# Optimization experiments

Measured on AMD Instinct MI355X. Metric: run time of the kernel, lower is better.

The kernel has to match this reference:

```python
import jax, jax.numpy as jnp
import numpy as np

# model dims
B_, S_, D_ = 2, 2048, 1024
D_STATE, EXPAND, HEADDIM, CHUNK, NGROUPS = 128, 2, 64, 64, 1
D_INNER = EXPAND * D_
NHEADS = D_INNER // HEADDIM  # 32 ssd heads
D_PROJ = 2 * D_INNER + 2 * NGROUPS * D_STATE + NHEADS  # 4384
H_, KV_, HD_ = 16, 4, 64  # attention heads / kv heads / head dim
ROPE_DIMS = 16
MLP_DIM = int(3.0 * D_)


def _rmsnorm(x, w=None, eps=1e-5):
    y = x * jax.lax.rsqrt(jnp.mean(x * x, axis=-1, keepdims=True) + eps)
    return y * w if w is not None else y


def _layernorm(x, w, b, eps=1e-5):
    m = jnp.mean(x, axis=-1, keepdims=True)
    v = jnp.mean((x - m) ** 2, axis=-1, keepdims=True)
    return (x - m) * jax.lax.rsqrt(v + eps) * w + b


def _segsum(x):
    # (..., T) -> (..., T, T) lower-tri cumulative sums, -inf above diag
    T = x.shape[-1]
    i = jnp.arange(T)
    xx = jnp.where(i[:, None] > i[None, :], jnp.broadcast_to(x[..., None], x.shape + (T,)), 0.0)
    s = jnp.cumsum(xx, axis=-2)
    return jnp.where(i[:, None] >= i[None, :], s, -jnp.inf)


def _ssd_chunked(x, A, B, C, chunk):
    # x:(b,s,h,p) A:(b,s,h) B,C:(b,s,g,n)
    b, s, h, p = x.shape
    g, n = B.shape[2], B.shape[3]
    if g < h:
        B = jnp.repeat(B, h // g, axis=2)
        C = jnp.repeat(C, h // g, axis=2)
    c = s // chunk
    x = x.reshape(b, c, chunk, h, p)
    A = A.reshape(b, c, chunk, h).transpose(0, 3, 1, 2)  # b h c l
    B = B.reshape(b, c, chunk, h, n)
    C = C.reshape(b, c, chunk, h, n)
    L = jnp.exp(_segsum(A))
    Y_diag = jnp.einsum('bclhn,bcshn,bhcls,bcshp->bclhp', C, B, L, x)
    A_cum = jnp.cumsum(A, axis=-1)
    decay_states = jnp.exp(A_cum[..., -1:] - A_cum)
    states = jnp.einsum('bclhn,bhcl,bclhp->bchpn', B, decay_states, x)
    decay_chunk = jnp.exp(_segsum(jnp.pad(A_cum[..., -1], ((0, 0), (0, 0), (1, 0)))))
    new_states = jnp.einsum('bhzc,bchpn->bzhpn', decay_chunk[:, :, :c, 1:c + 1], states)
    Y_off = jnp.einsum('bclhn,bchpn,bhcl->bclhp', C, new_states, jnp.exp(A_cum))
    return (Y_diag + Y_off).reshape(b, s, h, p)


def _rope_cos_sin(s, rd, base=10000.0):
    inv = 1.0 / base ** (jnp.arange(0, rd, 2, dtype=jnp.float32) / rd)
    f = jnp.outer(jnp.arange(s, dtype=jnp.float32), inv)  # (s, rd/2)
    return jnp.cos(f)[None, :, None, :], jnp.sin(f)[None, :, None, :]


def _apply_rope(x, cos, sin, rd):
    xr, xp = x[..., :rd], x[..., rd:]
    half = rd // 2
    x1, x2 = xr[..., :half], xr[..., half:]
    xr = jnp.concatenate([x1 * cos + x2 * sin, -x1 * sin + x2 * cos], axis=-1)
    return jnp.concatenate([xr, xp], axis=-1)


def _mamba_block(x, mnorm_w, in_w, out_w, Dp, dt_b, A_log, Bn_w, Cn_w):
    b, s, _ = x.shape
    h = _rmsnorm(x, mnorm_w)
    zxbcdt = h @ in_w.T
    z, xs, Bc, Cc, dt = jnp.split(
        zxbcdt,
        [D_INNER, 2 * D_INNER, 2 * D_INNER + NGROUPS * D_STATE, 2 * D_INNER + 2 * NGROUPS * D_STATE],
        axis=-1)
    dt = jax.nn.softplus(dt + dt_b)  # (b,s,nheads)
    A = -jnp.exp(A_log)  # (nheads,)
    xs = xs.reshape(b, s, NHEADS, HEADDIM)
    Bc = _rmsnorm(Bc.reshape(b, s, NGROUPS, D_STATE), Bn_w)
    Cc = _rmsnorm(Cc.reshape(b, s, NGROUPS, D_STATE), Cn_w)
    y = _ssd_chunked(xs * dt[..., None], A[None, None, :] * dt, Bc, Cc, CHUNK)
    y = y + xs * Dp[None, None, :, None]
    y = y * jax.nn.silu(z).reshape(b, s, NHEADS, HEADDIM)
    return x + y.reshape(b, s, D_INNER) @ out_w.T


def _attn_block(x, ln1_w, ln1_b, cq_w, ck_w, cv_w, cproj_w, q_gain, ln2_w, ln2_b, fc_w, proj_w):
    b, s, d = x.shape
    h = _layernorm(x, ln1_w, ln1_b)
    q = (h @ cq_w.T).reshape(b, s, H_, HD_)
    k = (h @ ck_w.T).reshape(b, s, KV_, HD_)
    v = (h @ cv_w.T).reshape(b, s, KV_, HD_)
    eps = jnp.finfo(x.dtype).eps
    q = _rmsnorm(q, eps=eps)
    k = _rmsnorm(k, eps=eps)
    cos, sin = _rope_cos_sin(s, ROPE_DIMS)
    q = _apply_rope(q, cos, sin, ROPE_DIMS)
    k = _apply_rope(k, cos, sin, ROPE_DIMS)
    q = q * q_gain[None, None, :, None]
    rep = H_ // KV_
    k = jnp.repeat(k, rep, axis=2)
    v = jnp.repeat(v, rep, axis=2)
    scores = jnp.einsum('bqhd,bkhd->bhqk', q, k) / np.float32(np.sqrt(HD_))
    i = jnp.arange(s)
    scores = jnp.where(i[:, None] >= i[None, :], scores, -jnp.inf)
    w = jax.nn.softmax(scores, axis=-1)
    y = jnp.einsum('bhqk,bkhd->bqhd', w, v).reshape(b, s, d)
    x = x + y @ cproj_w.T
    h = _layernorm(x, ln2_w, ln2_b)
    return x + jax.nn.silu(h @ fc_w.T) @ proj_w.T


def setup_inputs() -> dict:
    key = jax.random.key(0)
    ks = jax.random.split(key, 16)
    rn = lambda k, shp, sc=0.02: (jax.random.normal(k, shp, dtype=jnp.float32) * sc)
    return {
        'x': jax.random.normal(ks[0], (B_, S_, D_), dtype=jnp.float32),
        'mnorm_w': jnp.ones((D_,), jnp.float32),
        'in_proj_w': rn(ks[1], (D_PROJ, D_)),
        'out_proj_w': rn(ks[2], (D_, D_INNER)),
        'D_param': jnp.ones((NHEADS,), jnp.float32),
        'dt_bias': rn(ks[3], (NHEADS,), 0.1),
        'A_log': jnp.log(0.5 + jax.random.uniform(ks[4], (NHEADS,), dtype=jnp.float32) * 0.5),
        'Bn_w': jnp.ones((D_STATE,), jnp.float32),
        'Cn_w': jnp.ones((D_STATE,), jnp.float32),
        'ln1_w': jnp.ones((D_,), jnp.float32),
        'ln1_b': jnp.zeros((D_,), jnp.float32),
        'cq_w': rn(ks[5], (D_, D_)),
        'ck_w': rn(ks[6], (KV_ * HD_, D_)),
        'cv_w': rn(ks[7], (KV_ * HD_, D_)),
        'cproj_w': rn(ks[8], (D_, D_)),
        'q_gain': jnp.full((H_,), 5.25, jnp.float32),
        'ln2_w': jnp.ones((D_,), jnp.float32),
        'ln2_b': jnp.zeros((D_,), jnp.float32),
        'fc_w': rn(ks[9], (MLP_DIM, D_)),
        'proj_w': rn(ks[10], (D_, MLP_DIM)),
    }


def reference(x, mnorm_w, in_proj_w, out_proj_w, D_param, dt_bias, A_log, Bn_w, Cn_w,
              ln1_w, ln1_b, cq_w, ck_w, cv_w, cproj_w, q_gain, ln2_w, ln2_b, fc_w, proj_w):
    x = _mamba_block(x, mnorm_w, in_proj_w, out_proj_w, D_param, dt_bias, A_log, Bn_w, Cn_w)
    x = _attn_block(x, ln1_w, ln1_b, cq_w, ck_w, cv_w, cproj_w, q_gain, ln2_w, ln2_b, fc_w, proj_w)
    return x
```

## Files before the change

kernel.cpp:

```cpp
#include <hip/hip_runtime.h>
#include <hip/hip_bf16.h>
#include <math.h>

#define B_    2
#define S_    2048
#define D_    1024
#define DI    2048
#define NH    32
#define HD    64
#define DS    128
#define CH    64
#define NC    32
#define DP    4384
#define HATT  16
#define KVH   4
#define RD    16
#define MLP   3072
#define ROWS  (B_*S_)

typedef __bf16 bf16;
typedef __bf16 bf16x8 __attribute__((ext_vector_type(8)));
typedef __bf16 bf16x4 __attribute__((ext_vector_type(4)));
typedef float  f32x4  __attribute__((ext_vector_type(4)));

__device__ __forceinline__ void async_copy16(const void* g, void* l) {
  __builtin_amdgcn_global_load_lds(
      (const __attribute__((address_space(1))) unsigned int*)g,
      (__attribute__((address_space(3))) unsigned int*)l, 16, 0, 0);
}

__device__ __forceinline__ float waveReduceSum(float v) {
#pragma unroll
  for (int off = 32; off > 0; off >>= 1) v += __shfl_down(v, off, 64);
  return v;
}

template<int NW>
__device__ __forceinline__ float blockReduceSum(float v, float* sh) {
  v = waveReduceSum(v);
  int lane = threadIdx.x & 63, wid = threadIdx.x >> 6;
  if (lane == 0) sh[wid] = v;
  __syncthreads();
  float s = 0.f;
#pragma unroll
  for (int i = 0; i < NW; i++) s += sh[i];
  __syncthreads();
  return s;
}

struct CastSeg { const float* src; bf16* dst; int nval; int ntot; int blk0; };
struct CastArgs { CastSeg seg[8]; };

__global__ __launch_bounds__(256) void castw_all(CastArgs a) {
  int blk = blockIdx.x;
  int si = 0;
#pragma unroll
  for (int i = 1; i < 8; i++) if (blk >= a.seg[i].blk0) si = i;
  CastSeg s = a.seg[si];
  int i = ((blk - s.blk0) * 256 + threadIdx.x) * 4;
  if (i >= s.ntot) return;
  float4 v = {0.f, 0.f, 0.f, 0.f};
  if (i < s.nval) v = *(const float4*)(s.src + i);
  bf16x4 o;
  o[0] = (bf16)v.x; o[1] = (bf16)v.y; o[2] = (bf16)v.z; o[3] = (bf16)v.w;
  *(bf16x4*)(s.dst + i) = o;
}

__global__ __launch_bounds__(256) void rmsnorm_k(const float* __restrict__ x,
                                                 const float* __restrict__ w,
                                                 bf16* __restrict__ y, int n) {
  __shared__ float sh[4];
  size_t row = blockIdx.x;
  const float* xr = x + row * n;
  bf16* yr = y + row * n;
  float ss = 0.f;
  for (int i = threadIdx.x; i < n; i += 256) { float v = xr[i]; ss += v * v; }
  ss = blockReduceSum<4>(ss, sh);
  float inv = rsqrtf(ss / n + 1e-5f);
  for (int i = threadIdx.x; i < n; i += 256) yr[i] = (bf16)(xr[i] * inv * w[i]);
}

template<int ACT, typename OT>
__global__ __launch_bounds__(256) void gemm_mfma(const bf16* __restrict__ A,
                                                 const bf16* __restrict__ W,
                                                 const float* __restrict__ R,
                                                 OT* __restrict__ C,
                                                 int M, int N, int K) {
  __shared__ bf16 As[128 * 32];
  __shared__ bf16 Ws[128 * 32];
  int tid = threadIdx.x, lane = tid & 63, wave = tid >> 6;
  int bm = blockIdx.y * 128, bn = blockIdx.x * 128;
  const bf16* gA0 = A + (size_t)(bm + wave * 32 + (lane >> 2)) * K + (lane & 3) * 8;
  const bf16* gA1 = gA0 + (size_t)16 * K;
  const bf16* gW0 = W + (size_t)(bn + wave * 32 + (lane >> 2)) * K + (lane & 3) * 8;
  const bf16* gW1 = gW0 + (size_t)16 * K;
  bf16* lA0 = As + wave * 32 * 32;
  bf16* lA1 = lA0 + 16 * 32;
  bf16* lW0 = Ws + wave * 32 * 32;
  bf16* lW1 = lW0 + 16 * 32;
  int fr = lane & 15, fq = lane >> 4;
  int wm = wave >> 1, wn = wave & 1;
  const bf16* pA = As + (wm * 64 + fr) * 32 + fq * 8;
  const bf16* pW = Ws + (wn * 64 + fr) * 32 + fq * 8;
  f32x4 acc[4][4] = {};
  for (int k0 = 0; k0 < K; k0 += 32) {
    async_copy16(gA0, lA0);
    async_copy16(gA1, lA1);
    async_copy16(gW0, lW0);
    async_copy16(gW1, lW1);
    gA0 += 32; gA1 += 32; gW0 += 32; gW1 += 32;
    __syncthreads();
    bf16x8 af[4], bfr[4];
#pragma unroll
    for (int mi = 0; mi < 4; mi++) af[mi] = *(const bf16x8*)(pA + mi * 16 * 32);
#pragma unroll
    for (int ni = 0; ni < 4; ni++) bfr[ni] = *(const bf16x8*)(pW + ni * 16 * 32);
#pragma unroll
    for (int mi = 0; mi < 4; mi++)
#pragma unroll
      for (int ni = 0; ni < 4; ni++)
        acc[mi][ni] = __builtin_amdgcn_mfma_f32_16x16x32_bf16(af[mi], bfr[ni], acc[mi][ni], 0, 0, 0);
    __syncthreads();
  }
#pragma unroll
  for (int mi = 0; mi < 4; mi++) {
    int row = bm + wm * 64 + mi * 16 + fq * 4;
#pragma unroll
    for (int ni = 0; ni < 4; ni++) {
      int col = bn + wn * 64 + ni * 16 + fr;
      if (col < N) {
#pragma unroll
        for (int r = 0; r < 4; r++) {
          float v = acc[mi][ni][r];
          if (ACT == 1) v = v / (1.f + __expf(-v));
          if (R) v += R[(size_t)(row + r) * N + col];
          C[(size_t)(row + r) * N + col] = (OT)v;
        }
      }
    }
  }
}

__global__ __launch_bounds__(256) void gemm_sk(const bf16* __restrict__ A,
                                               const bf16* __restrict__ W,
                                               float* __restrict__ P,
                                               int M, int N, int K, int kchunk) {
  __shared__ bf16 As[128 * 32];
  __shared__ bf16 Ws[128 * 32];
  int tid = threadIdx.x, lane = tid & 63, wave = tid >> 6;
  int bm = blockIdx.y * 128, bn = blockIdx.x * 128;
  int ks = blockIdx.z;
  int kbeg = ks * kchunk;
  const bf16* gA0 = A + (size_t)(bm + wave * 32 + (lane >> 2)) * K + kbeg + (lane & 3) * 8;
  const bf16* gA1 = gA0 + (size_t)16 * K;
  const bf16* gW0 = W + (size_t)(bn + wave * 32 + (lane >> 2)) * K + kbeg + (lane & 3) * 8;
  const bf16* gW1 = gW0 + (size_t)16 * K;
  bf16* lA0 = As + wave * 32 * 32;
  bf16* lA1 = lA0 + 16 * 32;
  bf16* lW0 = Ws + wave * 32 * 32;
  bf16* lW1 = lW0 + 16 * 32;
  int fr = lane & 15, fq = lane >> 4;
  int wm = wave >> 1, wn = wave & 1;
  const bf16* pA = As + (wm * 64 + fr) * 32 + fq * 8;
  const bf16* pW = Ws + (wn * 64 + fr) * 32 + fq * 8;
  f32x4 acc[4][4] = {};
  for (int k0 = 0; k0 < kchunk; k0 += 32) {
    async_copy16(gA0, lA0);
    async_copy16(gA1, lA1);
    async_copy16(gW0, lW0);
    async_copy16(gW1, lW1);
    gA0 += 32; gA1 += 32; gW0 += 32; gW1 += 32;
    __syncthreads();
    bf16x8 af[4], bfr[4];
#pragma unroll
    for (int mi = 0; mi < 4; mi++) af[mi] = *(const bf16x8*)(pA + mi * 16 * 32);
#pragma unroll
    for (int ni = 0; ni < 4; ni++) bfr[ni] = *(const bf16x8*)(pW + ni * 16 * 32);
#pragma unroll
    for (int mi = 0; mi < 4; mi++)
#pragma unroll
      for (int ni = 0; ni < 4; ni++)
        acc[mi][ni] = __builtin_amdgcn_mfma_f32_16x16x32_bf16(af[mi], bfr[ni], acc[mi][ni], 0, 0, 0);
    __syncthreads();
  }
  float* Pp = P + (size_t)ks * M * N;
#pragma unroll
  for (int mi = 0; mi < 4; mi++) {
    int row = bm + wm * 64 + mi * 16 + fq * 4;
#pragma unroll
    for (int ni = 0; ni < 4; ni++) {
      int col = bn + wn * 64 + ni * 16 + fr;
#pragma unroll
      for (int r = 0; r < 4; r++)
        Pp[(size_t)(row + r) * N + col] = acc[mi][ni][r];
    }
  }
}

__global__ __launch_bounds__(256) void reduce_ln2(const float* __restrict__ p0,
                                                  const float* __restrict__ p1,
                                                  const float* __restrict__ res,
                                                  const float* __restrict__ w,
                                                  const float* __restrict__ b,
                                                  float* __restrict__ xo,
                                                  bf16* __restrict__ ho) {
  __shared__ float buf[1024];
  __shared__ float sh[4];
  size_t o = (size_t)blockIdx.x * 1024;
  float s = 0.f, s2 = 0.f;
  for (int i = threadIdx.x; i < 1024; i += 256) {
    float v = p0[o + i] + p1[o + i] + res[o + i];
    buf[i] = v; s += v; s2 += v * v;
  }
  s  = blockReduceSum<4>(s,  sh);
  s2 = blockReduceSum<4>(s2, sh);
  float mean = s / 1024.f;
  float var  = s2 / 1024.f - mean * mean;
  float inv  = rsqrtf(var + 1e-5f);
  for (int i = threadIdx.x; i < 1024; i += 256) {
    float v = buf[i];
    xo[o + i] = v;
    ho[o + i] = (bf16)((v - mean) * inv * w[i] + b[i]);
  }
}

__global__ __launch_bounds__(256) void reduce_out3(const float* __restrict__ p0,
                                                   const float* __restrict__ p1,
                                                   const float* __restrict__ p2,
                                                   const float* __restrict__ res,
                                                   float* __restrict__ out) {
  int i = (blockIdx.x * 256 + threadIdx.x) * 4;
  f32x4 v = *(const f32x4*)(p0 + i);
  v += *(const f32x4*)(p1 + i);
  v += *(const f32x4*)(p2 + i);
  v += *(const f32x4*)(res + i);
  *(f32x4*)(out + i) = v;
}

__global__ __launch_bounds__(256) void reduce_qkv(const float* __restrict__ P,
                                                  const float* __restrict__ q_gain,
                                                  bf16* __restrict__ q,
                                                  bf16* __restrict__ k,
                                                  bf16* __restrict__ v) {
  __shared__ float buf[1536];
  size_t row = blockIdx.x;
  size_t o = row * 1536;
  const float* p0 = P + o;
  const float* p1 = P + (size_t)ROWS * 1536 + o;
  int tid = threadIdx.x;
  for (int i = tid; i < 384; i += 256) {
    f32x4 a = *(const f32x4*)(p0 + i * 4);
    f32x4 c = *(const f32x4*)(p1 + i * 4);
    *(f32x4*)(buf + i * 4) = a + c;
  }
  __syncthreads();
  int lane = tid & 63, w = tid >> 6;
  int s = (int)(row & (S_ - 1));
  int ri = lane & 7;
  float rinv = __expf(-(float)ri * (0.125f * 9.210340371976184f));
  float ang = (float)s * rinv;
  float cs = cosf(ang), sn = sinf(ang);
#pragma unroll
  for (int j = 0; j < 6; j++) {
    int hh = w * 6 + j;
    float val = buf[hh * 64 + lane];
    if (hh < 20) {
      float ss = val * val;
#pragma unroll
      for (int off = 32; off > 0; off >>= 1) ss += __shfl_xor(ss, off, 64);
      val *= rsqrtf(ss / 64.f + 1.1920929e-7f);
      float other = __shfl_xor(val, 8, 64);
      float res = val;
      if (lane < RD) res = (lane < 8) ? (val * cs + other * sn) : (val * cs - other * sn);
      if (hh < 16) {
        res *= q_gain[hh];
        q[row * (HATT * HD) + hh * HD + lane] = (bf16)res;
      } else {
        k[row * (KVH * HD) + (hh - 16) * HD + lane] = (bf16)res;
      }
    } else {
      v[row * (KVH * HD) + (hh - 20) * HD + lane] = (bf16)val;
    }
  }
}

__global__ __launch_bounds__(256) void gemm_inproj(const bf16* __restrict__ A,
                                                   const bf16* __restrict__ W,
                                                   bf16* __restrict__ zt,
                                                   bf16* __restrict__ xt,
                                                   bf16* __restrict__ bcdt) {
  const int K = 1024;
  __shared__ bf16 As[128 * 32];
  __shared__ bf16 Ws[128 * 32];
  int tid = threadIdx.x, lane = tid & 63, wave = tid >> 6;
  int bm = blockIdx.y * 128, bn = blockIdx.x * 128;
  const bf16* gA0 = A + (size_t)(bm + wave * 32 + (lane >> 2)) * K + (lane & 3) * 8;
  const bf16* gA1 = gA0 + (size_t)16 * K;
  const bf16* gW0 = W + (size_t)(bn + wave * 32 + (lane >> 2)) * K + (lane & 3) * 8;
  const bf16* gW1 = gW0 + (size_t)16 * K;
  bf16* lA0 = As + wave * 32 * 32;
  bf16* lA1 = lA0 + 16 * 32;
  bf16* lW0 = Ws + wave * 32 * 32;
  bf16* lW1 = lW0 + 16 * 32;
  int fr = lane & 15, fq = lane >> 4;
  int wm = wave >> 1, wn = wave & 1;
  const bf16* pA = As + (wm * 64 + fr) * 32 + fq * 8;
  const bf16* pW = Ws + (wn * 64 + fr) * 32 + fq * 8;
  f32x4 acc[4][4] = {};
  for (int k0 = 0; k0 < K; k0 += 32) {
    async_copy16(gA0, lA0);
    async_copy16(gA1, lA1);
    async_copy16(gW0, lW0);
    async_copy16(gW1, lW1);
    gA0 += 32; gA1 += 32; gW0 += 32; gW1 += 32;
    __syncthreads();
    bf16x8 af[4], bfr[4];
#pragma unroll
    for (int mi = 0; mi < 4; mi++) af[mi] = *(const bf16x8*)(pA + mi * 16 * 32);
#pragma unroll
    for (int ni = 0; ni < 4; ni++) bfr[ni] = *(const bf16x8*)(pW + ni * 16 * 32);
#pragma unroll
    for (int mi = 0; mi < 4; mi++)
#pragma unroll
      for (int ni = 0; ni < 4; ni++)
        acc[mi][ni] = __builtin_amdgcn_mfma_f32_16x16x32_bf16(af[mi], bfr[ni], acc[mi][ni], 0, 0, 0);
    __syncthreads();
  }
#pragma unroll
  for (int mi = 0; mi < 4; mi++) {
    int row0m = bm + wm * 64 + mi * 16 + fq * 4;
    int b = row0m >> 11, sg = row0m & 2047;
#pragma unroll
    for (int ni = 0; ni < 4; ni++) {
      int col = bn + wn * 64 + ni * 16 + fr;
      bf16x4 o;
#pragma unroll
      for (int r = 0; r < 4; r++) o[r] = (bf16)acc[mi][ni][r];
      if (col < 2048) {
        *(bf16x4*)(zt + ((size_t)(b * NH + (col >> 6)) * HD + (col & 63)) * S_ + sg) = o;
      } else if (col < 4096) {
        int xc = col - 2048;
        *(bf16x4*)(xt + ((size_t)(b * NH + (xc >> 6)) * HD + (xc & 63)) * S_ + sg) = o;
      } else if (col < 4384) {
#pragma unroll
        for (int r = 0; r < 4; r++)
          bcdt[(size_t)(row0m + r) * 288 + (col - 4096)] = o[r];
      }
    }
  }
}

__global__ __launch_bounds__(256) void t64(const bf16* __restrict__ in, bf16* __restrict__ out,
                                           int istr, size_t io, size_t oo, int n_nt) {
  __shared__ bf16 T[64 * 72];
  int bid = blockIdx.x;
  int st = bid & 31;
  int nt = (bid >> 5) % n_nt;
  int outer = bid / (32 * n_nt);
  const bf16* ip = in + outer * io + (size_t)st * 64 * istr + nt * 64;
  int tid = threadIdx.x;
#pragma unroll
  for (int i = 0; i < 2; i++) {
    int cid = tid + i * 256; int s = cid >> 3, pc = (cid & 7) * 8;
    *(bf16x8*)(T + s * 72 + pc) = *(const bf16x8*)(ip + (size_t)s * istr + pc);
  }
  __syncthreads();
  bf16* op = out + outer * oo + (size_t)nt * 64 * 2048 + st * 64;
#pragma unroll
  for (int i = 0; i < 2; i++) {
    int cid = tid + i * 256; int p = cid >> 3, sc = (cid & 7) * 8;
    bf16x8 o;
#pragma unroll
    for (int j = 0; j < 8; j++) o[j] = T[(sc + j) * 72 + p];
    *(bf16x8*)(op + (size_t)p * 2048 + sc) = o;
  }
}

__global__ __launch_bounds__(64) void ssd_prep(const bf16* __restrict__ bcdt,
                                               const float* __restrict__ dt_bias,
                                               const float* __restrict__ A_log,
                                               float* __restrict__ dt_c,
                                               float* __restrict__ ddc,
                                               float* __restrict__ ac_c,
                                               float* __restrict__ T_out) {
  int bid = blockIdx.x;
  int c = bid % NC, hh = (bid / NC) % NH, b = bid / (NC * NH);
  int l = threadIdx.x;
  size_t row = (size_t)b * S_ + c * 64 + l;
  float raw = (float)bcdt[row * 288 + 256 + hh] + dt_bias[hh];
  float dtv = (raw > 20.f) ? raw : log1pf(__expf(raw));
  float a = -__expf(A_log[hh]) * dtv;
  float ps = a;
#pragma unroll
  for (int off = 1; off < 64; off <<= 1) {
    float t = __shfl_up(ps, off, 64);
    if (l >= off) ps += t;
  }
  float a63 = __shfl(ps, 63, 64);
  size_t o = ((size_t)b * NH + hh) * S_ + c * 64 + l;
  dt_c[o] = dtv;
  ac_c[o] = ps;
  ddc[o] = __expf(a63 - ps) * dtv;
  if (l == 63) T_out[(b * NH + hh) * NC + c] = ps;
}

__global__ __launch_bounds__(128) void bc_norm(const bf16* __restrict__ bcdt,
                                               const float* __restrict__ Bw,
                                               const float* __restrict__ Cw,
                                               bf16* __restrict__ Bn,
                                               bf16* __restrict__ Cn) {
  __shared__ float shb[2], shc[2];
  size_t row = blockIdx.x;
  int i = threadIdx.x;
  float bv = (float)bcdt[row * 288 + i];
  float cv = (float)bcdt[row * 288 + 128 + i];
  float sb = waveReduceSum(bv * bv);
  float sc = waveReduceSum(cv * cv);
  int lane = threadIdx.x & 63, wid = threadIdx.x >> 6;
  if (lane == 0) { shb[wid] = sb; shc[wid] = sc; }
  __syncthreads();
  float tb = shb[0] + shb[1];
  float tc = shc[0] + shc[1];
  Bn[row * DS + i] = (bf16)(bv * rsqrtf(tb / DS + 1e-5f) * Bw[i]);
  Cn[row * DS + i] = (bf16)(cv * rsqrtf(tc / DS + 1e-5f) * Cw[i]);
}

__global__ __launch_bounds__(256) void ssd_states(const bf16* __restrict__ Xt,
                                                  const bf16* __restrict__ Btr,
                                                  const float* __restrict__ ddc,
                                                  float* __restrict__ states) {
  __shared__ bf16 Xs[64 * 72];
  __shared__ bf16 Bs[128 * 72];
  int bid = blockIdx.x;
  int h = bid % NH;
  int c = (bid / NH) % NC;
  int b = bid / (NH * NC);
  int tid = threadIdx.x, lane = tid & 63, w = tid >> 6;
  int fr = lane & 15, fq = lane >> 4;
  const size_t xbase = (size_t)(b * NH + h) * HD * S_ + c * 64;
  const size_t dbase = (size_t)(b * NH + h) * S_ + c * 64;
#pragma unroll
  for (int i = 0; i < 2; i++) {
    int cid = tid + i * 256; int p = cid >> 3, sc = (cid & 7) * 8;
    bf16x8 xv = *(const bf16x8*)(Xt + xbase + (size_t)p * S_ + sc);
    f32x4 d0 = *(const f32x4*)(ddc + dbase + sc);
    f32x4 d1 = *(const f32x4*)(ddc + dbase + sc + 4);
    bf16x8 o;
#pragma unroll
    for (int j = 0; j < 4; j++) { o[j] = (bf16)((float)xv[j] * d0[j]); o[4 + j] = (bf16)((float)xv[4 + j] * d1[j]); }
    *(bf16x8*)(Xs + p * 72 + sc) = o;
  }
  const size_t bbase = (size_t)b * 128 * S_ + c * 64;
#pragma unroll
  for (int i = 0; i < 4; i++) {
    int cid = tid + i * 256; int n = cid >> 3, sc = (cid & 7) * 8;
    *(bf16x8*)(Bs + n * 72 + sc) = *(const bf16x8*)(Btr + bbase + (size_t)n * S_ + sc);
  }
  __syncthreads();
  f32x4 acc[4][2] = {};
#pragma unroll
  for (int ks = 0; ks < 2; ks++) {
    bf16x8 a[4], bb[2];
#pragma unroll
    for (int pt = 0; pt < 4; pt++) a[pt] = *(const bf16x8*)(Xs + (pt * 16 + fr) * 72 + ks * 32 + fq * 8);
#pragma unroll
    for (int n2 = 0; n2 < 2; n2++) bb[n2] = *(const bf16x8*)(Bs + ((2 * w + n2) * 16 + fr) * 72 + ks * 32 + fq * 8);
#pragma unroll
    for (int pt = 0; pt < 4; pt++)
#pragma unroll
      for (int n2 = 0; n2 < 2; n2++)
        acc[pt][n2] = __builtin_amdgcn_mfma_f32_16x16x32_bf16(a[pt], bb[n2], acc[pt][n2], 0, 0, 0);
  }
  float* outp = states + (size_t)bid * 8192;
#pragma unroll
  for (int pt = 0; pt < 4; pt++)
#pragma unroll
    for (int n2 = 0; n2 < 2; n2++) {
      int n = (2 * w + n2) * 16 + fr;
#pragma unroll
      for (int r = 0; r < 4; r++)
        outp[(size_t)(pt * 16 + fq * 4 + r) * 128 + n] = acc[pt][n2][r];
    }
}

__global__ __launch_bounds__(256) void ssd_scan(float* __restrict__ states,
                                                const float* __restrict__ T) {
  __shared__ float eT[NC];
  int part = blockIdx.x & 7;
  int bh = blockIdx.x >> 3;
  int b = bh / NH, h = bh % NH;
  if (threadIdx.x < NC) eT[threadIdx.x] = __expf(T[(size_t)(b * NH + h) * NC + threadIdx.x]);
  __syncthreads();
  const size_t cstride = (size_t)NH * HD * DS;
  size_t base = ((size_t)b * NC * NH + h) * (HD * DS);
#pragma unroll
  for (int j = 0; j < 4; j++) {
    int e = part * 1024 + threadIdx.x + j * 256;
    float carry = 0.f;
    size_t idx = base + e;
    for (int c = 0; c < NC; c++) {
      float sv = states[idx];
      states[idx] = carry;
      carry = sv + eT[c] * carry;
      idx += cstride;
    }
  }
}

__global__ __launch_bounds__(256) void ssd_out(const bf16* __restrict__ Cn,
                                               const bf16* __restrict__ Bn,
                                               const bf16* __restrict__ Xt,
                                               const bf16* __restrict__ Zt,
                                               const float* __restrict__ dt_c,
                                               const float* __restrict__ ac_c,
                                               const float* __restrict__ states,
                                               const float* __restrict__ Dp,
                                               bf16* __restrict__ ybf) {
  __shared__ bf16 Cs[64 * 136];
  __shared__ bf16 BNs[64 * 136];
  __shared__ bf16 Xs[64 * 72];
  __shared__ bf16 G[64 * 72];
  __shared__ float acs[64];
  int bid = blockIdx.x;
  int h = bid % NH;
  int c = (bid / NH) % NC;
  int b = bid / (NH * NC);
  int tid = threadIdx.x, lane = tid & 63, w = tid >> 6;
  int fr = lane & 15, fq = lane >> 4;
  size_t row0 = (size_t)b * S_ + c * 64;
  const size_t abase = (size_t)(b * NH + h) * S_ + c * 64;
  if (tid < 64) acs[tid] = ac_c[abase + tid];
#pragma unroll
  for (int i = 0; i < 4; i++) {
    int cid = tid + i * 256; int l = cid >> 4, nc = (cid & 15) * 8;
    float e = __expf(ac_c[abase + l]);
    bf16x8 cv = *(const bf16x8*)(Cn + (row0 + l) * DS + nc);
    bf16x8 o;
#pragma unroll
    for (int j = 0; j < 8; j++) o[j] = (bf16)((float)cv[j] * e);
    *(bf16x8*)(Cs + l * 136 + nc) = o;
    *(bf16x8*)(BNs + l * 136 + nc) = *(const bf16x8*)(Bn + (row0 + l) * DS + nc);
  }
  const size_t xbase = (size_t)(b * NH + h) * HD * S_ + c * 64;
#pragma unroll
  for (int i = 0; i < 2; i++) {
    int cid = tid + i * 256; int p = cid >> 3, sc = (cid & 7) * 8;
    bf16x8 xv = *(const bf16x8*)(Xt + xbase + (size_t)p * S_ + sc);
    f32x4 d0 = *(const f32x4*)(dt_c + abase + sc);
    f32x4 d1 = *(const f32x4*)(dt_c + abase + sc + 4);
    bf16x8 o;
#pragma unroll
    for (int j = 0; j < 4; j++) { o[j] = (bf16)((float)xv[j] * d0[j]); o[4 + j] = (bf16)((float)xv[4 + j] * d1[j]); }
    *(bf16x8*)(Xs + p * 72 + sc) = o;
  }
  __syncthreads();
  bf16x8 ca[4];
#pragma unroll
  for (int ks = 0; ks < 4; ks++) ca[ks] = *(const bf16x8*)(Cs + (w * 16 + fr) * 136 + ks * 32 + fq * 8);
  f32x4 cb[4] = {};
  for (int st = 0; st <= w; st++)
#pragma unroll
    for (int ks = 0; ks < 4; ks++)
      cb[st] = __builtin_amdgcn_mfma_f32_16x16x32_bf16(ca[ks],
                 *(const bf16x8*)(BNs + (st * 16 + fr) * 136 + ks * 32 + fq * 8), cb[st], 0, 0, 0);
#pragma unroll
  for (int st = 0; st < 4; st++) {
    float es = (st <= w) ? __expf(-acs[st * 16 + fr]) : 0.f;
#pragma unroll
    for (int r = 0; r < 4; r++) {
      int lloc = fq * 4 + r;
      float g = 0.f;
      if (st < w) g = cb[st][r] * es;
      else if (st == w) g = (lloc >= fr) ? cb[st][r] * es : 0.f;
      G[(w * 16 + lloc) * 72 + st * 16 + fr] = (bf16)g;
    }
  }
  f32x4 acc[4] = {};
  {
    bf16x8 ga0 = *(const bf16x8*)(G + (w * 16 + fr) * 72 + fq * 8);
    bf16x8 ga1 = *(const bf16x8*)(G + (w * 16 + fr) * 72 + 32 + fq * 8);
#pragma unroll
    for (int pt = 0; pt < 4; pt++) {
      acc[pt] = __builtin_amdgcn_mfma_f32_16x16x32_bf16(ga0,
                  *(const bf16x8*)(Xs + (pt * 16 + fr) * 72 + fq * 8), acc[pt], 0, 0, 0);
      acc[pt] = __builtin_amdgcn_mfma_f32_16x16x32_bf16(ga1,
                  *(const bf16x8*)(Xs + (pt * 16 + fr) * 72 + 32 + fq * 8), acc[pt], 0, 0, 0);
    }
  }
  __syncthreads();
  const float* stp = states + (size_t)bid * 8192;
#pragma unroll
  for (int i = 0; i < 4; i++) {
    int cid = tid + i * 256; int p = cid >> 4, nc = (cid & 15) * 8;
    f32x4 s0 = *(const f32x4*)(stp + (size_t)p * 128 + nc);
    f32x4 s1 = *(const f32x4*)(stp + (size_t)p * 128 + nc + 4);
    bf16x8 o;
#pragma unroll
    for (int j = 0; j < 4; j++) { o[j] = (bf16)s0[j]; o[4 + j] = (bf16)s1[j]; }
    *(bf16x8*)(BNs + p * 136 + nc) = o;
  }
  __syncthreads();
#pragma unroll
  for (int pt = 0; pt < 4; pt++)
#pragma unroll
    for (int ks = 0; ks < 4; ks++)
      acc[pt] = __builtin_amdgcn_mfma_f32_16x16x32_bf16(ca[ks],
                  *(const bf16x8*)(BNs + (pt * 16 + fr) * 136 + ks * 32 + fq * 8), acc[pt], 0, 0, 0);
  float dph = Dp[h];
#pragma unroll
  for (int pt = 0; pt < 4; pt++) {
    int p = pt * 16 + fr;
    size_t tb = (xbase + (size_t)p * S_) + w * 16 + fq * 4;
    bf16x4 xs4 = *(const bf16x4*)(Xt + tb);
    bf16x4 z4  = *(const bf16x4*)(Zt + tb);
#pragma unroll
    for (int r = 0; r < 4; r++) {
      int l = w * 16 + fq * 4 + r;
      float yv = acc[pt][r] + (float)xs4[r] * dph;
      float z = (float)z4[r];
      yv *= z / (1.f + __expf(-z));
      ybf[((row0 + l) * NH + h) * HD + p] = (bf16)yv;
    }
  }
}

#define KSTR 72
#define PSTR 80
__global__ __launch_bounds__(256) void attn_mfma(const bf16* __restrict__ q,
                                                 const bf16* __restrict__ k,
                                                 const bf16* __restrict__ vtr,
                                                 bf16* __restrict__ o) {
  __shared__ bf16 Ks[2][64 * KSTR];
  __shared__ bf16 Vs[2][64 * KSTR];
  __shared__ bf16 Pl[4 * 16 * PSTR];
  int qt = (gridDim.x - 1) - blockIdx.x;
  int h = blockIdx.y, b = blockIdx.z;
  int kvh = h >> 2;
  int tid = threadIdx.x, lane = tid & 63, w = tid >> 6;
  int fr = lane & 15, fq = lane >> 4;
  const float SC = 0.18033688011112042f;
  const float M2 = 62.0f;
  const bf16* qp = q + (size_t)(b * S_ + qt * 64 + w * 16 + fr) * (HATT * HD) + h * HD + fq * 8;
  bf16x8 bq0 = *(const bf16x8*)(qp);
  bf16x8 bq1 = *(const bf16x8*)(qp + 32);
  int sr = tid >> 3, sc8 = (tid & 7) * 8;
  const bf16* kg = k + ((size_t)(b * S_) + sr) * (KVH * HD) + kvh * HD + sc8;
  const bf16* vg = vtr + ((size_t)(b * KVH + kvh) * HD + sr) * S_ + sc8;
  bf16x8 krg0, krg1, vrg0, vrg1;
  {
    const bf16* kp = kg;
    const bf16* vp = vg;
    krg0 = *(const bf16x8*)(kp);
    krg1 = *(const bf16x8*)(kp + (size_t)32 * (KVH * HD));
    vrg0 = *(const bf16x8*)(vp);
    vrg1 = *(const bf16x8*)(vp + (size_t)32 * S_);
    *(bf16x8*)(&Ks[0][sr * KSTR + sc8]) = krg0;
    *(bf16x8*)(&Ks[0][(sr + 32) * KSTR + sc8]) = krg1;
    *(bf16x8*)(&Vs[0][sr * KSTR + sc8]) = vrg0;
    *(bf16x8*)(&Vs[0][(sr + 32) * KSTR + sc8]) = vrg1;
  }
  float lsum = 0.f;
  f32x4 yacc[4] = {};
  bf16* Plw = Pl + w * 16 * PSTR;
  for (int kt = 0; kt <= qt; kt++) {
    int cur = kt & 1;
    bool more = kt < qt;
    if (more) {
      const bf16* kp = kg + (size_t)(kt + 1) * 64 * (KVH * HD);
      const bf16* vp = vg + (size_t)(kt + 1) * 64;
      krg0 = *(const bf16x8*)(kp);
      krg1 = *(const bf16x8*)(kp + (size_t)32 * (KVH * HD));
      vrg0 = *(const bf16x8*)(vp);
      vrg1 = *(const bf16x8*)(vp + (size_t)32 * S_);
    }
    __syncthreads();
    bool diag = (kt == qt);
#pragma unroll
    for (int mi = 0; mi < 4; mi++) {
      bf16x4 pk = {};
      if (!diag || mi <= w) {
        const bf16* krow = &Ks[cur][(mi * 16 + fr) * KSTR + fq * 8];
        bf16x8 ak0 = *(const bf16x8*)(krow);
        bf16x8 ak1 = *(const bf16x8*)(krow + 32);
        f32x4 s = {};
        s = __builtin_amdgcn_mfma_f32_16x16x32_bf16(ak0, bq0, s, 0, 0, 0);
        s = __builtin_amdgcn_mfma_f32_16x16x32_bf16(ak1, bq1, s, 0, 0, 0);
#pragma unroll
        for (int r = 0; r < 4; r++) {
          bool ok = !diag || (mi < w) || (fq * 4 + r <= fr);
          float p = ok ? __builtin_amdgcn_exp2f(s[r] * SC - M2) : 0.f;
          lsum += p;
          pk[r] = (bf16)p;
        }
      }
      *(bf16x4*)(Plw + fr * PSTR + mi * 16 + fq * 4) = pk;
    }
    bf16x8 bp0 = *(const bf16x8*)(Plw + fr * PSTR + fq * 8);
    bool hi = !diag || (w >= 2);
    bf16x8 bp1 = {};
    if (hi) bp1 = *(const bf16x8*)(Plw + fr * PSTR + 32 + fq * 8);
#pragma unroll
    for (int pi = 0; pi < 4; pi++) {
      const bf16* vrow = &Vs[cur][(pi * 16 + fr) * KSTR + fq * 8];
      bf16x8 av0 = *(const bf16x8*)(vrow);
      yacc[pi] = __builtin_amdgcn_mfma_f32_16x16x32_bf16(av0, bp0, yacc[pi], 0, 0, 0);
      if (hi) {
        bf16x8 av1 = *(const bf16x8*)(vrow + 32);
        yacc[pi] = __builtin_amdgcn_mfma_f32_16x16x32_bf16(av1, bp1, yacc[pi], 0, 0, 0);
      }
    }
    if (more) {
      int nxt = cur ^ 1;
      *(bf16x8*)(&Ks[nxt][sr * KSTR + sc8]) = krg0;
      *(bf16x8*)(&Ks[nxt][(sr + 32) * KSTR + sc8]) = krg1;
      *(bf16x8*)(&Vs[nxt][sr * KSTR + sc8]) = vrg0;
      *(bf16x8*)(&Vs[nxt][(sr + 32) * KSTR + sc8]) = vrg1;
    }
  }
  lsum += __shfl_xor(lsum, 16, 64);
  lsum += __shfl_xor(lsum, 32, 64);
  float inv = 1.f / lsum;
  bf16* op = o + (size_t)(b * S_ + qt * 64 + w * 16 + fr) * (HATT * HD) + h * HD + fq * 4;
#pragma unroll
  for (int pi = 0; pi < 4; pi++) {
    bf16x4 ov;
#pragma unroll
    for (int r = 0; r < 4; r++) ov[r] = (bf16)(yacc[pi][r] * inv);
    *(bf16x4*)(op + pi * 16) = ov;
  }
}

constexpr size_t OFF_WIN  = 0;
constexpr size_t OFF_WOUT = 9175040;
constexpr size_t OFF_WQKV = 13369344;
constexpr size_t OFF_WCP  = 16515072;
constexpr size_t OFF_WFC  = 18612224;
constexpr size_t OFF_WPR  = 24903680;
constexpr size_t OFF_HBF  = 31195136;
constexpr size_t OFF_BCDT = 39583744;
constexpr size_t OFF_XT   = 41943040;
constexpr size_t OFF_ZT   = 58720256;
constexpr size_t OFF_DTC  = 75497472;
constexpr size_t OFF_DDC  = 76546048;
constexpr size_t OFF_ACC  = 77594624;
constexpr size_t OFF_T    = 78643200;
constexpr size_t OFF_BN   = 78651392;
constexpr size_t OFF_CN   = 79699968;
constexpr size_t OFF_BTR  = 80748544;
constexpr size_t OFF_ST   = 81797120;
constexpr size_t OFF_YBF  = 148905984;
constexpr size_t OFF_X1   = 165683200;
constexpr size_t OFF_P    = OFF_ST;
constexpr size_t OFF_QB   = OFF_ST + 50331648;
constexpr size_t OFF_KB   = OFF_ST + 58720256;
constexpr size_t OFF_VB   = OFF_ST + 60817408;
constexpr size_t OFF_VTR  = OFF_ST + 62914560;
constexpr size_t OFF_Y2   = OFF_XT;
constexpr size_t OFF_X2   = 50331648;
constexpr size_t OFF_MLP  = 132128768;

extern "C" void kernel_launch(void* const* d_in, const int* in_sizes, int n_in,
                              void* d_out, int out_size, void* d_ws, size_t ws_size,
                              hipStream_t stream) {
  (void)in_sizes; (void)n_in; (void)out_size; (void)ws_size;
  const float* x        = (const float*)d_in[0];
  const float* mnorm_w  = (const float*)d_in[1];
  const float* in_w     = (const float*)d_in[2];
  const float* out_w    = (const float*)d_in[3];
  const float* Dp       = (const float*)d_in[4];
  const float* dt_bias  = (const float*)d_in[5];
  const float* A_log    = (const float*)d_in[6];
  const float* Bn_w     = (const float*)d_in[7];
  const float* Cn_w     = (const float*)d_in[8];
  const float* ln1_w    = (const float*)d_in[9];
  const float* ln1_b    = (const float*)d_in[10];
  const float* cq_w     = (const float*)d_in[11];
  const float* ck_w     = (const float*)d_in[12];
  const float* cv_w     = (const float*)d_in[13];
  const float* cproj_w  = (const float*)d_in[14];
  const float* q_gain   = (const float*)d_in[15];
  const float* ln2_w    = (const float*)d_in[16];
  const float* ln2_b    = (const float*)d_in[17];
  const float* fc_w     = (const float*)d_in[18];
  const float* proj_w   = (const float*)d_in[19];
  float* out = (float*)d_out;
  char* W8 = (char*)d_ws;

  bf16* w_in   = (bf16*)(W8 + OFF_WIN);
  bf16* w_out  = (bf16*)(W8 + OFF_WOUT);
  bf16* w_qkv  = (bf16*)(W8 + OFF_WQKV);
  bf16* w_cp   = (bf16*)(W8 + OFF_WCP);
  bf16* w_fc   = (bf16*)(W8 + OFF_WFC);
  bf16* w_pr   = (bf16*)(W8 + OFF_WPR);
  bf16* h_bf   = (bf16*)(W8 + OFF_HBF);
  bf16* bcdt   = (bf16*)(W8 + OFF_BCDT);
  bf16* Xt     = (bf16*)(W8 + OFF_XT);
  bf16* Zt     = (bf16*)(W8 + OFF_ZT);
  float* dt_c  = (float*)(W8 + OFF_DTC);
  float* ddc   = (float*)(W8 + OFF_DDC);
  float* ac_c  = (float*)(W8 + OFF_ACC);
  float* Tb    = (float*)(W8 + OFF_T);
  bf16* Bn     = (bf16*)(W8 + OFF_BN);
  bf16* Cn     = (bf16*)(W8 + OFF_CN);
  bf16* Btr    = (bf16*)(W8 + OFF_BTR);
  float* st    = (float*)(W8 + OFF_ST);
  bf16* ybf    = (bf16*)(W8 + OFF_YBF);
  float* x1    = (float*)(W8 + OFF_X1);
  float* Pbuf  = (float*)(W8 + OFF_P);
  bf16* qbf    = (bf16*)(W8 + OFF_QB);
  bf16* kbf    = (bf16*)(W8 + OFF_KB);
  bf16* vbf    = (bf16*)(W8 + OFF_VB);
  bf16* vtr    = (bf16*)(W8 + OFF_VTR);
  bf16* y2     = (bf16*)(W8 + OFF_Y2);
  float* x2    = (float*)(W8 + OFF_X2);
  bf16* mlp    = (bf16*)(W8 + OFF_MLP);

  CastArgs ca;
  ca.seg[0] = { in_w,    w_in,            4489216, 4587520, 0     };
  ca.seg[1] = { out_w,   w_out,           2097152, 2097152, 4480  };
  ca.seg[2] = { cq_w,    w_qkv,           1048576, 1048576, 6528  };
  ca.seg[3] = { ck_w,    w_qkv + 1048576,  262144,  262144, 7552  };
  ca.seg[4] = { cv_w,    w_qkv + 1310720,  262144,  262144, 7808  };
  ca.seg[5] = { cproj_w, w_cp,            1048576, 1048576, 8064  };
  ca.seg[6] = { fc_w,    w_fc,            3145728, 3145728, 9088  };
  ca.seg[7] = { proj_w,  w_pr,            3145728, 3145728, 12160 };
  castw_all<<<15232, 256, 0, stream>>>(ca);

  const size_t PS = (size_t)ROWS * 1024;

  rmsnorm_k<<<ROWS, 256, 0, stream>>>(x, mnorm_w, h_bf, D_);
  gemm_inproj<<<dim3(35, 32), 256, 0, stream>>>(h_bf, w_in, Zt, Xt, bcdt);
  ssd_prep<<<B_ * NH * NC, 64, 0, stream>>>(bcdt, dt_bias, A_log, dt_c, ddc, ac_c, Tb);
  bc_norm<<<ROWS, 128, 0, stream>>>(bcdt, Bn_w, Cn_w, Bn, Cn);
  t64<<<2 * 2 * 32, 256, 0, stream>>>(Bn, Btr, 128, (size_t)2048 * 128, (size_t)128 * 2048, 2);
  ssd_states<<<B_ * NC * NH, 256, 0, stream>>>(Xt, Btr, ddc, st);
  ssd_scan<<<B_ * NH * 8, 256, 0, stream>>>(st, Tb);
  ssd_out<<<B_ * NC * NH, 256, 0, stream>>>(Cn, Bn, Xt, Zt, dt_c, ac_c, st, Dp, ybf);
  gemm_sk<<<dim3(8, 32, 2), 256, 0, stream>>>(ybf, w_out, Pbuf, ROWS, D_, DI, 1024);
  reduce_ln2<<<ROWS, 256, 0, stream>>>(Pbuf, Pbuf + PS, x, ln1_w, ln1_b, x1, h_bf);

  gemm_sk<<<dim3(12, 32, 2), 256, 0, stream>>>(h_bf, w_qkv, Pbuf, ROWS, 1536, D_, 512);
  reduce_qkv<<<ROWS, 256, 0, stream>>>(Pbuf, q_gain, qbf, kbf, vbf);
  t64<<<2 * 4 * 32, 256, 0, stream>>>(vbf, vtr, 256, (size_t)2048 * 256, (size_t)256 * 2048, 4);
  attn_mfma<<<dim3(S_ / 64, HATT, B_), 256, 0, stream>>>(qbf, kbf, vtr, y2);
  gemm_sk<<<dim3(8, 32, 2), 256, 0, stream>>>(y2, w_cp, Pbuf, ROWS, D_, D_, 512);
  reduce_ln2<<<ROWS, 256, 0, stream>>>(Pbuf, Pbuf + PS, x1, ln2_w, ln2_b, x2, h_bf);

  gemm_mfma<1, bf16><<<dim3(24, 32), 256, 0, stream>>>(h_bf, w_fc, nullptr, mlp, ROWS, MLP, D_);
  gemm_sk<<<dim3(8, 32, 3), 256, 0, stream>>>(mlp, w_pr, Pbuf, ROWS, D_, MLP, 1024);
  reduce_out3<<<ROWS, 256, 0, stream>>>(Pbuf, Pbuf + PS, Pbuf + 2 * PS, x2, out);
}
```

Before: 609.6 us.

## Store SSD chunk states in bf16 and enlarge attention query tile to 128

The SSD chunk-state buffer moves from fp32 to bf16. That halves the traffic through ssd_states, ssd_scan and ssd_out and removes the fp32-to-bf16 conversion in ssd_out, but each scan step now rounds the carried state to bf16, which can lose precision. Separately, the attention kernel now gives each block 128 queries (32 per wave, two 16-row subtiles), so every K/V tile loaded into LDS is reused across twice as many queries and the grid is halved. Causal masking becomes per-element and fully masked subtiles are zero-filled.

After: 574.9 us. 5.7% less time.

```diff
diff --git a/kernel.cpp b/kernel.cpp
--- a/kernel.cpp
+++ b/kernel.cpp
@@ -428,7 +428,7 @@
 __global__ __launch_bounds__(256) void ssd_states(const bf16* __restrict__ Xt,
                                                   const bf16* __restrict__ Btr,
                                                   const float* __restrict__ ddc,
-                                                  float* __restrict__ states) {
+                                                  bf16* __restrict__ states) {
   __shared__ bf16 Xs[64 * 72];
   __shared__ bf16 Bs[128 * 72];
   int bid = blockIdx.x;
@@ -471,7 +471,7 @@
       for (int n2 = 0; n2 < 2; n2++)
         acc[pt][n2] = __builtin_amdgcn_mfma_f32_16x16x32_bf16(a[pt], bb[n2], acc[pt][n2], 0, 0, 0);
   }
-  float* outp = states + (size_t)bid * 8192;
+  bf16* outp = states + (size_t)bid * 8192;
 #pragma unroll
   for (int pt = 0; pt < 4; pt++)
 #pragma unroll
@@ -479,11 +479,11 @@
       int n = (2 * w + n2) * 16 + fr;
 #pragma unroll
       for (int r = 0; r < 4; r++)
-        outp[(size_t)(pt * 16 + fq * 4 + r) * 128 + n] = acc[pt][n2][r];
-    }
-}
-
-__global__ __launch_bounds__(256) void ssd_scan(float* __restrict__ states,
+        outp[(size_t)(pt * 16 + fq * 4 + r) * 128 + n] = (bf16)acc[pt][n2][r];
+    }
+}
+
+__global__ __launch_bounds__(256) void ssd_scan(bf16* __restrict__ states,
                                                 const float* __restrict__ T) {
   __shared__ float eT[NC];
   int part = blockIdx.x & 7;
@@ -499,8 +499,8 @@
     float carry = 0.f;
     size_t idx = base + e;
     for (int c = 0; c < NC; c++) {
-      float sv = states[idx];
-      states[idx] = carry;
+      float sv = (float)states[idx];
+      states[idx] = (bf16)carry;
       carry = sv + eT[c] * carry;
       idx += cstride;
     }
@@ -513,7 +513,7 @@
                                                const bf16* __restrict__ Zt,
                                                const float* __restrict__ dt_c,
                                                const float* __restrict__ ac_c,
-                                               const float* __restrict__ states,
+                                               const bf16* __restrict__ states,
                                                const float* __restrict__ Dp,
                                                bf16* __restrict__ ybf) {
   __shared__ bf16 Cs[64 * 136];
@@ -588,16 +588,11 @@
     }
   }
   __syncthreads();
-  const float* stp = states + (size_t)bid * 8192;
+  const bf16* stp = states + (size_t)bid * 8192;
 #pragma unroll
   for (int i = 0; i < 4; i++) {
     int cid = tid + i * 256; int p = cid >> 4, nc = (cid & 15) * 8;
-    f32x4 s0 = *(const f32x4*)(stp + (size_t)p * 128 + nc);
-    f32x4 s1 = *(const f32x4*)(stp + (size_t)p * 128 + nc + 4);
-    bf16x8 o;
-#pragma unroll
-    for (int j = 0; j < 4; j++) { o[j] = (bf16)s0[j]; o[4 + j] = (bf16)s1[j]; }
-    *(bf16x8*)(BNs + p * 136 + nc) = o;
+    *(bf16x8*)(BNs + p * 136 + nc) = *(const bf16x8*)(stp + (size_t)p * 128 + nc);
   }
   __syncthreads();
 #pragma unroll
@@ -625,14 +620,14 @@
 }
 
 #define KSTR 72
-#define PSTR 80
+#define PSTR 72
 __global__ __launch_bounds__(256) void attn_mfma(const bf16* __restrict__ q,
                                                  const bf16* __restrict__ k,
                                                  const bf16* __restrict__ vtr,
                                                  bf16* __restrict__ o) {
   __shared__ bf16 Ks[2][64 * KSTR];
   __shared__ bf16 Vs[2][64 * KSTR];
-  __shared__ bf16 Pl[4 * 16 * PSTR];
+  __shared__ bf16 Pl[4][32 * PSTR];
   int qt = (gridDim.x - 1) - blockIdx.x;
   int h = blockIdx.y, b = blockIdx.z;
   int kvh = h >> 2;
@@ -640,31 +635,36 @@
   int fr = lane & 15, fq = lane >> 4;
   const float SC = 0.18033688011112042f;
   const float M2 = 62.0f;
-  const bf16* qp = q + (size_t)(b * S_ + qt * 64 + w * 16 + fr) * (HATT * HD) + h * HD + fq * 8;
-  bf16x8 bq0 = *(const bf16x8*)(qp);
-  bf16x8 bq1 = *(const bf16x8*)(qp + 32);
+  int qbase = qt * 128 + w * 32;
+  int qmaxw = qbase + 31;
+  bf16x8 bq[2][2];
+#pragma unroll
+  for (int qc = 0; qc < 2; qc++)
+#pragma unroll
+    for (int ks = 0; ks < 2; ks++)
+      bq[qc][ks] = *(const bf16x8*)(q + (size_t)(b * S_ + qbase + qc * 16 + fr) * (HATT * HD)
+                                      + h * HD + ks * 32 + fq * 8);
   int sr = tid >> 3, sc8 = (tid & 7) * 8;
   const bf16* kg = k + ((size_t)(b * S_) + sr) * (KVH * HD) + kvh * HD + sc8;
   const bf16* vg = vtr + ((size_t)(b * KVH + kvh) * HD + sr) * S_ + sc8;
   bf16x8 krg0, krg1, vrg0, vrg1;
   {
-    const bf16* kp = kg;
-    const bf16* vp = vg;
-    krg0 = *(const bf16x8*)(kp);
-    krg1 = *(const bf16x8*)(kp + (size_t)32 * (KVH * HD));
-    vrg0 = *(const bf16x8*)(vp);
-    vrg1 = *(const bf16x8*)(vp + (size_t)32 * S_);
+    krg0 = *(const bf16x8*)(kg);
+    krg1 = *(const bf16x8*)(kg + (size_t)32 * (KVH * HD));
+    vrg0 = *(const bf16x8*)(vg);
+    vrg1 = *(const bf16x8*)(vg + (size_t)32 * S_);
     *(bf16x8*)(&Ks[0][sr * KSTR + sc8]) = krg0;
     *(bf16x8*)(&Ks[0][(sr + 32) * KSTR + sc8]) = krg1;
     *(bf16x8*)(&Vs[0][sr * KSTR + sc8]) = vrg0;
     *(bf16x8*)(&Vs[0][(sr + 32) * KSTR + sc8]) = vrg1;
   }
-  float lsum = 0.f;
-  f32x4 yacc[4] = {};
-  bf16* Plw = Pl + w * 16 * PSTR;
-  for (int kt = 0; kt <= qt; kt++) {
+  float lsum[2] = {0.f, 0.f};
+  f32x4 yacc[2][4] = {};
+  bf16* Plw = Pl[w];
+  int nkt = 2 * qt + 2;
+  for (int kt = 0; kt < nkt; kt++) {
     int cur = kt & 1;
-    bool more = kt < qt;
+    bool more = (kt + 1) < nkt;
     if (more) {
       const bf16* kp = kg + (size_t)(kt + 1) * 64 * (KVH * HD);
       const bf16* vp = vg + (size_t)(kt + 1) * 64;
@@ -674,39 +674,50 @@
       vrg1 = *(const bf16x8*)(vp + (size_t)32 * S_);
     }
     __syncthreads();
-    bool diag = (kt == qt);
-#pragma unroll
-    for (int mi = 0; mi < 4; mi++) {
-      bf16x4 pk = {};
-      if (!diag || mi <= w) {
-        const bf16* krow = &Ks[cur][(mi * 16 + fr) * KSTR + fq * 8];
-        bf16x8 ak0 = *(const bf16x8*)(krow);
-        bf16x8 ak1 = *(const bf16x8*)(krow + 32);
-        f32x4 s = {};
-        s = __builtin_amdgcn_mfma_f32_16x16x32_bf16(ak0, bq0, s, 0, 0, 0);
-        s = __builtin_amdgcn_mfma_f32_16x16x32_bf16(ak1, bq1, s, 0, 0, 0);
-#pragma unroll
-        for (int r = 0; r < 4; r++) {
-          bool ok = !diag || (mi < w) || (fq * 4 + r <= fr);
-          float p = ok ? __builtin_amdgcn_exp2f(s[r] * SC - M2) : 0.f;
-          lsum += p;
-          pk[r] = (bf16)p;
+    if (kt * 64 <= qmaxw) {
+#pragma unroll
+      for (int mi = 0; mi < 4; mi++) {
+        int s0 = kt * 64 + mi * 16;
+        if (s0 > qmaxw) {
+          bf16x4 zz = {};
+#pragma unroll
+          for (int qc = 0; qc < 2; qc++)
+            *(bf16x4*)(Plw + (qc * 16 + fr) * PSTR + mi * 16 + fq * 4) = zz;
+        } else {
+          const bf16* krow = &Ks[cur][(mi * 16 + fr) * KSTR];
+          bf16x8 ak0 = *(const bf16x8*)(krow + fq * 8);
+          bf16x8 ak1 = *(const bf16x8*)(krow + 32 + fq * 8);
+#pragma unroll
+          for (int qc = 0; qc < 2; qc++) {
+            f32x4 s = {};
+            s = __builtin_amdgcn_mfma_f32_16x16x32_bf16(ak0, bq[qc][0], s, 0, 0, 0);
+            s = __builtin_amdgcn_mfma_f32_16x16x32_bf16(ak1, bq[qc][1], s, 0, 0, 0);
+            int qq = qbase + qc * 16 + fr;
+            bf16x4 pk;
+#pragma unroll
+            for (int r = 0; r < 4; r++) {
+              int sp = s0 + fq * 4 + r;
+              float p = (sp <= qq) ? __builtin_amdgcn_exp2f(s[r] * SC - M2) : 0.f;
+              lsum[qc] += p;
+              pk[r] = (bf16)p;
+            }
+            *(bf16x4*)(Plw + (qc * 16 + fr) * PSTR + mi * 16 + fq * 4) = pk;
+          }
         }
       }
-      *(bf16x4*)(Plw + fr * PSTR + mi * 16 + fq * 4) = pk;
-    }
-    bf16x8 bp0 = *(const bf16x8*)(Plw + fr * PSTR + fq * 8);
-    bool hi = !diag || (w >= 2);
-    bf16x8 bp1 = {};
-    if (hi) bp1 = *(const bf16x8*)(Plw + fr * PSTR + 32 + fq * 8);
-#pragma unroll
-    for (int pi = 0; pi < 4; pi++) {
-      const bf16* vrow = &Vs[cur][(pi * 16 + fr) * KSTR + fq * 8];
-      bf16x8 av0 = *(const bf16x8*)(vrow);
-      yacc[pi] = __builtin_amdgcn_mfma_f32_16x16x32_bf16(av0, bp0, yacc[pi], 0, 0, 0);
-      if (hi) {
-        bf16x8 av1 = *(const bf16x8*)(vrow + 32);
-        yacc[pi] = __builtin_amdgcn_mfma_f32_16x16x32_bf16(av1, bp1, yacc[pi], 0, 0, 0);
+#pragma unroll
+      for (int ks2 = 0; ks2 < 2; ks2++) {
+        bf16x8 bp[2];
+#pragma unroll
+        for (int qc = 0; qc < 2; qc++)
+          bp[qc] = *(const bf16x8*)(Plw + (qc * 16 + fr) * PSTR + ks2 * 32 + fq * 8);
+#pragma unroll
+        for (int pi = 0; pi < 4; pi++) {
+          bf16x8 av = *(const bf16x8*)(&Vs[cur][(pi * 16 + fr) * KSTR + ks2 * 32 + fq * 8]);
+#pragma unroll
+          for (int qc = 0; qc < 2; qc++)
+            yacc[qc][pi] = __builtin_amdgcn_mfma_f32_16x16x32_bf16(av, bp[qc], yacc[qc][pi], 0, 0, 0);
+        }
       }
     }
     if (more) {
@@ -717,16 +728,22 @@
       *(bf16x8*)(&Vs[nxt][(sr + 32) * KSTR + sc8]) = vrg1;
     }
   }
-  lsum += __shfl_xor(lsum, 16, 64);
-  lsum += __shfl_xor(lsum, 32, 64);
-  float inv = 1.f / lsum;
-  bf16* op = o + (size_t)(b * S_ + qt * 64 + w * 16 + fr) * (HATT * HD) + h * HD + fq * 4;
-#pragma unroll
-  for (int pi = 0; pi < 4; pi++) {
-    bf16x4 ov;
-#pragma unroll
-    for (int r = 0; r < 4; r++) ov[r] = (bf16)(yacc[pi][r] * inv);
-    *(bf16x4*)(op + pi * 16) = ov;
+#pragma unroll
+  for (int qc = 0; qc < 2; qc++) {
+    lsum[qc] += __shfl_xor(lsum[qc], 16, 64);
+    lsum[qc] += __shfl_xor(lsum[qc], 32, 64);
+  }
+#pragma unroll
+  for (int qc = 0; qc < 2; qc++) {
+    float inv = 1.f / lsum[qc];
+    bf16* op = o + (size_t)(b * S_ + qbase + qc * 16 + fr) * (HATT * HD) + h * HD + fq * 4;
+#pragma unroll
+    for (int pi = 0; pi < 4; pi++) {
+      bf16x4 ov;
+#pragma unroll
+      for (int r = 0; r < 4; r++) ov[r] = (bf16)(yacc[qc][pi][r] * inv);
+      *(bf16x4*)(op + pi * 16) = ov;
+    }
   }
 }
 
@@ -803,7 +820,7 @@
   bf16* Bn     = (bf16*)(W8 + OFF_BN);
   bf16* Cn     = (bf16*)(W8 + OFF_CN);
   bf16* Btr    = (bf16*)(W8 + OFF_BTR);
-  float* st    = (float*)(W8 + OFF_ST);
+  bf16* st     = (bf16*)(W8 + OFF_ST);
   bf16* ybf    = (bf16*)(W8 + OFF_YBF);
   float* x1    = (float*)(W8 + OFF_X1);
   float* Pbuf  = (float*)(W8 + OFF_P);
@@ -842,7 +859,7 @@
   gemm_sk<<<dim3(12, 32, 2), 256, 0, stream>>>(h_bf, w_qkv, Pbuf, ROWS, 1536, D_, 512);
   reduce_qkv<<<ROWS, 256, 0, stream>>>(Pbuf, q_gain, qbf, kbf, vbf);
   t64<<<2 * 4 * 32, 256, 0, stream>>>(vbf, vtr, 256, (size_t)2048 * 256, (size_t)256 * 2048, 4);
-  attn_mfma<<<dim3(S_ / 64, HATT, B_), 256, 0, stream>>>(qbf, kbf, vtr, y2);
+  attn_mfma<<<dim3(S_ / 128, HATT, B_), 256, 0, stream>>>(qbf, kbf, vtr, y2);
   gemm_sk<<<dim3(8, 32, 2), 256, 0, stream>>>(y2, w_cp, Pbuf, ROWS, D_, D_, 512);
   reduce_ln2<<<ROWS, 256, 0, stream>>>(Pbuf, Pbuf + PS, x1, ln2_w, ln2_b, x2, h_bf);
 
```
